# Kernel tuning notes

Measured on AMD Instinct MI355X. Metric: run time of the kernel, lower is better.

Reference implementation:

```python
import jax, jax.numpy as jnp
import numpy as np

N, E, G = 50000, 800000, 128          # nodes, edges, graphs
L, T, F = 4, 4, 20                    # conv layers, towers, per-tower width
D = T * F                             # 80 = hidden dim
EDGE_DIM = 16
AVG_DEG_LOG = float(np.log(17.0))     # avg_deg['log'] for avg in-degree ~16
EPS_STD = 1e-5
EPS_BN = 1e-5


def setup_inputs() -> dict:
    ks = iter(jax.random.split(jax.random.key(0), 32))
    rn = lambda *s: jax.random.normal(next(ks), s, jnp.float32) * 0.1
    return dict(
        x=jax.random.randint(next(ks), (N, 9), 0, 16),
        edge_index=jax.random.randint(next(ks), (2, E), 0, N),
        batch=jnp.sort(jax.random.randint(next(ks), (N,), 0, G)),
        edge_attr=rn(E, EDGE_DIM),
        atom_emb=rn(9, 16, D),
        edge_w=rn(L, EDGE_DIM, F), edge_b=jnp.zeros((L, F), jnp.float32),
        pre_w1=rn(L, T, 3 * F, F), pre_b1=jnp.zeros((L, T, F), jnp.float32),
        pre_w2=rn(L, T, F, F), pre_b2=jnp.zeros((L, T, F), jnp.float32),
        post_w1=rn(L, T, 13 * F, F), post_b1=jnp.zeros((L, T, F), jnp.float32),
        post_w2=rn(L, T, F, F), post_b2=jnp.zeros((L, T, F), jnp.float32),
        lin_w=rn(L, D, D), lin_b=jnp.zeros((L, D), jnp.float32),
        bn_g=jnp.ones((L, D), jnp.float32), bn_b=jnp.zeros((L, D), jnp.float32),
        mlp_w1=rn(D, 40), mlp_b1=jnp.zeros(40, jnp.float32),
        mlp_w2=rn(40, 20), mlp_b2=jnp.zeros(20, jnp.float32),
        mlp_w3=rn(20, 1), mlp_b3=jnp.zeros(1, jnp.float32),
    )


def _net(x, edge_index, batch, edge_attr, atom_emb, edge_w, edge_b, pre_w1,
         pre_b1, pre_w2, pre_b2, post_w1, post_b1, post_w2, post_b2, lin_w,
         lin_b, bn_g, bn_b, mlp_w1, mlp_b1, mlp_w2, mlp_b2, mlp_w3, mlp_b3):
    src, dst = edge_index[0], edge_index[1]
    # AtomEncoder: sum of 9 categorical embeddings -> [N, D]
    h = atom_emb[jnp.arange(9)[None, :], x].sum(1)
    deg_raw = jax.ops.segment_sum(jnp.ones((E,), jnp.float32), dst, N)
    deg = jnp.clip(deg_raw, 1.0)
    has_edge = (deg_raw > 0)[:, None, None]
    d3 = deg[:, None, None]
    logd = jnp.log(deg + 1.0)[:, None, None]
    for l in range(L):  # 4 PNAConv + BN + ReLU + residual (dropout off / eval)
        xt = h.reshape(N, T, F)
        ea = edge_attr @ edge_w[l] + edge_b[l]                      # [E, F]
        # message: concat(x_i, x_j, edge) -> per-tower pre MLP
        m = jnp.concatenate([xt[dst], xt[src],
                             jnp.broadcast_to(ea[:, None, :], (E, T, F))], -1)
        m = jax.nn.relu(jnp.einsum('eti,tio->eto', m, pre_w1[l]) + pre_b1[l])
        m = jnp.einsum('eti,tio->eto', m, pre_w2[l]) + pre_b2[l]    # [E,T,F]
        # multi-aggregator scatter-reduce
        mean = jax.ops.segment_sum(m, dst, N) / d3
        msq = jax.ops.segment_sum(m * m, dst, N) / d3
        std = jnp.sqrt(jax.nn.relu(msq - mean * mean) + EPS_STD)
        mn = jnp.where(has_edge, jax.ops.segment_min(m, dst, N), 0.0)
        mx = jnp.where(has_edge, jax.ops.segment_max(m, dst, N), 0.0)
        agg = jnp.concatenate([mean, mn, mx, std], -1)              # [N,T,4F]
        # degree scalers: identity, amplification, attenuation
        out = jnp.concatenate([agg, agg * (logd / AVG_DEG_LOG),
                               agg * (AVG_DEG_LOG / logd)], -1)     # [N,T,12F]
        out = jnp.concatenate([xt, out], -1)                        # [N,T,13F]
        out = jax.nn.relu(jnp.einsum('nti,tio->nto', out, post_w1[l]) + post_b1[l])
        out = jnp.einsum('nti,tio->nto', out, post_w2[l]) + post_b2[l]
        out = out.reshape(N, D) @ lin_w[l] + lin_b[l]
        # BatchNorm over nodes (batch statistics)
        mu = out.mean(0)
        var = jnp.mean((out - mu) ** 2, axis=0)
        out = (out - mu) * (bn_g[l] / jnp.sqrt(var + EPS_BN)) + bn_b[l]
        h = jax.nn.relu(out) + h
    # global mean pool over graphs + readout MLP
    cnt = jnp.clip(jax.ops.segment_sum(jnp.ones((N,), jnp.float32), batch, G), 1.0)
    g = jax.ops.segment_sum(h, batch, G) / cnt[:, None]
    g = jax.nn.relu(g @ mlp_w1 + mlp_b1)
    g = jax.nn.relu(g @ mlp_w2 + mlp_b2)
    return g @ mlp_w3 + mlp_b3                                      # [G, 1]


def reference(x, edge_index, batch, edge_attr, atom_emb, edge_w, edge_b, pre_w1,
              pre_b1, pre_w2, pre_b2, post_w1, post_b1, post_w2, post_b2, lin_w,
              lin_b, bn_g, bn_b, mlp_w1, mlp_b1, mlp_w2, mlp_b2, mlp_w3, mlp_b3):
    return _net(x, edge_index, batch, edge_attr, atom_emb, edge_w, edge_b, pre_w1,
                pre_b1, pre_w2, pre_b2, post_w1, post_b1, post_w2, post_b2,
                lin_w, lin_b, bn_g, bn_b, mlp_w1, mlp_b1, mlp_w2, mlp_b2,
                mlp_w3, mlp_b3)
```

## Files before the change

kernel.cpp:

```cpp
#include <hip/hip_runtime.h>
#include <hip/hip_bf16.h>

#define NN 50000
#define EE 800000
#define GG 128
#define LL 4
#define TT 4
#define FF 20
#define DD 80
#define SCAN_B ((NN + 1023) / 1024)
#define TILE_N 16
#define ITEMS (TILE_N * 10)
static constexpr float AVG_LOG = 2.8332133440562162f;

typedef __fp16 half2v __attribute__((ext_vector_type(2)));

__device__ __forceinline__ float bf2f(unsigned short u) {
  return __uint_as_float((unsigned)u << 16);
}
__device__ __forceinline__ unsigned short f2bf(float f) {
  __hip_bfloat16 b = __float2bfloat16(f);
  return *(unsigned short*)&b;
}
__device__ __forceinline__ half2v pkrtz(float a, float b) {
#if __has_builtin(__builtin_amdgcn_cvt_pkrtz)
  return __builtin_amdgcn_cvt_pkrtz(a, b);
#else
  half2v h; h.x = (__fp16)a; h.y = (__fp16)b; return h;
#endif
}
__device__ __forceinline__ float fdot2(half2v a, half2v b, float c) {
#if __has_builtin(__builtin_amdgcn_fdot2)
  return __builtin_amdgcn_fdot2(a, b, c, false);
#else
  return fmaf((float)a.x, (float)b.x, fmaf((float)a.y, (float)b.y, c));
#endif
}
__device__ __forceinline__ half2v u2h2(unsigned int u) {
  return __builtin_bit_cast(half2v, u);
}
__device__ __forceinline__ unsigned int h22u(half2v h) {
  return __builtin_bit_cast(unsigned int, h);
}
__device__ __forceinline__ unsigned int packh2_rne(float a, float b) {
  half2v h; h.x = (__fp16)a; h.y = (__fp16)b;
  return h22u(h);
}
__device__ __forceinline__ unsigned int pack_bf16(float a, float b) {
  return (unsigned int)f2bf(a) | ((unsigned int)f2bf(b) << 16);
}

__global__ __launch_bounds__(256) void k_h(const int* __restrict__ x,
                                           const float* __restrict__ atom_emb,
                                           float* __restrict__ h) {
  int idx = blockIdx.x * 256 + threadIdx.x;
  if (idx >= NN * DD) return;
  int n = idx / DD, d = idx - n * DD;
  const int* xr = x + n * 9;
  float acc = 0.f;
#pragma unroll
  for (int i = 0; i < 9; ++i) {
    int v = xr[i];
    acc += atom_emb[(i * 16 + v) * DD + d];
  }
  h[idx] = acc;
}

__global__ __launch_bounds__(256) void k_deg(const int* __restrict__ ei, int* __restrict__ cnt) {
  int e = blockIdx.x * 256 + threadIdx.x;
  if (e >= EE) return;
  atomicAdd(&cnt[ei[EE + e]], 1);
}

__global__ __launch_bounds__(1024) void k_scan_sum(const int* __restrict__ cnt, int* __restrict__ bsum) {
  __shared__ int red[1024];
  int tid = threadIdx.x;
  int i = blockIdx.x * 1024 + tid;
  red[tid] = (i < NN) ? cnt[i] : 0;
  __syncthreads();
  for (int off = 512; off > 0; off >>= 1) {
    if (tid < off) red[tid] += red[tid + off];
    __syncthreads();
  }
  if (tid == 0) bsum[blockIdx.x] = red[0];
}

__global__ void k_scan_top(const int* __restrict__ bsum, int* __restrict__ boff,
                           int* __restrict__ row_ptr) {
  if (threadIdx.x == 0 && blockIdx.x == 0) {
    int acc = 0;
    for (int b = 0; b < SCAN_B; ++b) { boff[b] = acc; acc += bsum[b]; }
    row_ptr[NN] = acc;
  }
}

__global__ __launch_bounds__(1024) void k_scan_apply(const int* __restrict__ cnt,
                                                     const int* __restrict__ boff,
                                                     int* __restrict__ row_ptr,
                                                     int* __restrict__ cursor) {
  __shared__ int sm[1024];
  int tid = threadIdx.x;
  int i = blockIdx.x * 1024 + tid;
  int v = (i < NN) ? cnt[i] : 0;
  sm[tid] = v;
  __syncthreads();
  for (int off = 1; off < 1024; off <<= 1) {
    int t = (tid >= off) ? sm[tid - off] : 0;
    __syncthreads();
    sm[tid] += t;
    __syncthreads();
  }
  int excl = boff[blockIdx.x] + sm[tid] - v;
  if (i < NN) { row_ptr[i] = excl; cursor[i] = excl; }
}

__global__ __launch_bounds__(256) void k_csrfill(const int* __restrict__ ei,
                                                 int* __restrict__ cursor,
                                                 int* __restrict__ csr_src,
                                                 int* __restrict__ csr_eid,
                                                 int* __restrict__ csr_dst) {
  int e = blockIdx.x * 256 + threadIdx.x;
  if (e >= EE) return;
  int dst = ei[EE + e];
  int slot = atomicAdd(&cursor[dst], 1);
  csr_src[slot] = ei[e];
  csr_eid[slot] = e;
  csr_dst[slot] = dst;
}

__global__ __launch_bounds__(256) void k_eagather(const int* __restrict__ csr_eid,
                                                  const float* __restrict__ edge_attr,
                                                  unsigned int* __restrict__ ea16) {
  int sl = blockIdx.x * 256 + threadIdx.x;
  if (sl >= EE) return;
  int e = csr_eid[sl];
  const float4* ap = (const float4*)(edge_attr + (size_t)e * 16);
  uint4 o0, o1;
  float4 v0 = ap[0], v1 = ap[1], v2 = ap[2], v3 = ap[3];
  o0.x = packh2_rne(v0.x, v0.y); o0.y = packh2_rne(v0.z, v0.w);
  o0.z = packh2_rne(v1.x, v1.y); o0.w = packh2_rne(v1.z, v1.w);
  o1.x = packh2_rne(v2.x, v2.y); o1.y = packh2_rne(v2.z, v2.w);
  o1.z = packh2_rne(v3.x, v3.y); o1.w = packh2_rne(v3.z, v3.w);
  uint4* op = (uint4*)(ea16 + (size_t)sl * 8);
  op[0] = o0; op[1] = o1;
}

__global__ __launch_bounds__(256) void k_nodeparams(const int* __restrict__ cnt,
                                                    float* __restrict__ inv_deg,
                                                    float* __restrict__ s1a,
                                                    float* __restrict__ s2a) {
  int n = blockIdx.x * 256 + threadIdx.x;
  if (n >= NN) return;
  int c = cnt[n];
  float deg = (c > 0) ? (float)c : 1.0f;
  inv_deg[n] = 1.0f / deg;
  float logd = logf(deg + 1.0f);
  s1a[n] = logd / AVG_LOG;
  s2a[n] = AVG_LOG / logd;
}

__global__ __launch_bounds__(64) void k_wcomb(const float* __restrict__ edge_w,
                                              const float* __restrict__ edge_b,
                                              const float* __restrict__ pre_w1,
                                              const float* __restrict__ pre_b1,
                                              const float* __restrict__ pre_w2,
                                              unsigned int* __restrict__ wcpk,
                                              unsigned int* __restrict__ w2pk,
                                              float* __restrict__ biasc, int l) {
  int t = blockIdx.x;
  int wt = l * TT + t;
  const float* W1 = pre_w1 + (size_t)wt * 1200;
  const float* W2 = pre_w2 + (size_t)wt * 400;
  const float* ew = edge_w + (size_t)l * 16 * FF;
  const float* eb = edge_b + (size_t)l * FF;
  int j = threadIdx.x;
  if (j >= FF) return;
  float col[16];
  for (int i = 0; i < 16; ++i) {
    float acc = 0.f;
#pragma unroll
    for (int f = 0; f < FF; ++f) acc = fmaf(ew[i * FF + f], W1[(40 + f) * FF + j], acc);
    col[i] = acc;
  }
#pragma unroll
  for (int i2 = 0; i2 < 8; ++i2)
    wcpk[((size_t)t * FF + j) * 8 + i2] = packh2_rne(col[2 * i2], col[2 * i2 + 1]);
#pragma unroll
  for (int i2 = 0; i2 < 10; ++i2)
    w2pk[((size_t)t * FF + j) * 10 + i2] = packh2_rne(W2[(2 * i2) * FF + j], W2[(2 * i2 + 1) * FF + j]);
  float b = pre_b1[wt * FF + j];
#pragma unroll
  for (int f = 0; f < FF; ++f) b = fmaf(eb[f], W1[(40 + f) * FF + j], b);
  biasc[t * FF + j] = b;
}

__global__ __launch_bounds__(64) void k_postpk(const float* __restrict__ post_w1,
                                               const float* __restrict__ post_w2,
                                               unsigned int* __restrict__ q1pk,
                                               unsigned int* __restrict__ q2pk, int l) {
  int t = blockIdx.x;
  int wt = l * TT + t;
  const float* Q1 = post_w1 + (size_t)wt * 5200;
  const float* Q2 = post_w2 + (size_t)wt * 400;
  int j = threadIdx.x;
  if (j >= FF) return;
  for (int i2 = 0; i2 < 120; ++i2) {
    int blk = i2 / 40, k = i2 - blk * 40;
    int r0 = 20 + 80 * blk + 2 * k;
    q1pk[((size_t)t * 120 + i2) * FF + j] = packh2_rne(Q1[r0 * FF + j], Q1[(r0 + 1) * FF + j]);
  }
#pragma unroll
  for (int i2 = 0; i2 < 10; ++i2)
    q2pk[((size_t)t * 10 + i2) * FF + j] = packh2_rne(Q2[(2 * i2) * FF + j], Q2[(2 * i2 + 1) * FF + j]);
}

__global__ __launch_bounds__(256) void k_prenode(
    const float* __restrict__ h, const float* __restrict__ pre_w1,
    const float* __restrict__ biasc,
    unsigned short* __restrict__ predD, unsigned short* __restrict__ predS, int l) {
  int tid = threadIdx.x;
  int t = tid >> 6, lane = tid & 63;
  int n = blockIdx.x * 64 + lane;
  if (n >= NN) return;
  int wt_u = __builtin_amdgcn_readfirstlane(l * TT + t);
  const float* W1 = pre_w1 + (size_t)wt_u * 1200;
  const float* bc = biasc + t * FF;
  float xt[FF];
  {
    const float4* pp = (const float4*)(h + (size_t)n * DD + t * FF);
#pragma unroll
    for (int i = 0; i < 5; ++i) { float4 v = pp[i]; xt[i*4]=v.x; xt[i*4+1]=v.y; xt[i*4+2]=v.z; xt[i*4+3]=v.w; }
  }
  float d[FF], s[FF];
#pragma unroll
  for (int j = 0; j < FF; ++j) { d[j] = bc[j]; s[j] = 0.f; }
#pragma unroll
  for (int i = 0; i < FF; ++i) {
    float a = xt[i];
#pragma unroll
    for (int j = 0; j < FF; ++j) {
      d[j] = fmaf(a, W1[i * FF + j], d[j]);
      s[j] = fmaf(a, W1[(FF + i) * FF + j], s[j]);
    }
  }
  ushort4* pd = (ushort4*)(predD + (size_t)n * DD + t * FF);
  ushort4* ps = (ushort4*)(predS + (size_t)n * DD + t * FF);
#pragma unroll
  for (int i = 0; i < 5; ++i) {
    pd[i] = make_ushort4(f2bf(d[i*4]), f2bf(d[i*4+1]), f2bf(d[i*4+2]), f2bf(d[i*4+3]));
    ps[i] = make_ushort4(f2bf(s[i*4]), f2bf(s[i*4+1]), f2bf(s[i*4+2]), f2bf(s[i*4+3]));
  }
}

__global__ __launch_bounds__(256, 4) void k_preagg(
    const unsigned short* __restrict__ predD,
    const unsigned short* __restrict__ predS,
    const unsigned int* __restrict__ ea16,
    const int* __restrict__ csr_src,
    const int* __restrict__ csr_dst,
    const int* __restrict__ row_ptr,
    const float* __restrict__ inv_deg,
    const unsigned int* __restrict__ wcpk,
    const unsigned int* __restrict__ w2pk,
    const float* __restrict__ pre_b2,
    unsigned short* __restrict__ aggbuf,
    int l) {
  __shared__ int nbr[TILE_N + 1];
  __shared__ float dDs[TT][TILE_N * FF];
  __shared__ unsigned int m2w[TT][64 * 11];
  int tid = threadIdx.x;
  int t = tid >> 6, lane = tid & 63;
  int t_u = __builtin_amdgcn_readfirstlane(t);
  int n0 = blockIdx.x * TILE_N;
  const unsigned int* Wcp = wcpk + (size_t)t_u * FF * 8;
  const unsigned int* W2p = w2pk + (size_t)t_u * FF * 10;
  const float* b2 = pre_b2 + (size_t)(l * TT + t_u) * FF;

  if (tid <= TILE_N) {
    int node = n0 + tid; if (node > NN) node = NN;
    nbr[tid] = row_ptr[node];
  }
  for (int i = lane; i < TILE_N * FF; i += 64) {
    int ni = i / FF, ch = i - ni * FF;
    int node = n0 + ni;
    dDs[t][i] = (node < NN) ? bf2f(predD[(size_t)node * DD + t_u * FF + ch]) : 0.f;
  }
  __syncthreads();
  int tbeg = nbr[0], tend = nbr[TILE_N];

  int itN[3], itP[3], itB[3], itE[3];
#pragma unroll
  for (int k = 0; k < 3; ++k) {
    int it = lane + 64 * k;
    bool v = it < ITEMS;
    int nd = v ? (it / 10) : 0;
    itN[k] = nd;
    itP[k] = v ? (it - nd * 10) : 0;
    itB[k] = v ? nbr[nd] : 0;
    itE[k] = v ? nbr[nd + 1] : 0;
  }
  float sS[3][2], sQ[3][2], sN[3][2], sX[3][2];
#pragma unroll
  for (int k = 0; k < 3; ++k) {
    sS[k][0] = 0.f; sS[k][1] = 0.f; sQ[k][0] = 0.f; sQ[k][1] = 0.f;
    sN[k][0] = 3.4e38f; sN[k][1] = 3.4e38f; sX[k][0] = -3.4e38f; sX[k][1] = -3.4e38f;
  }

  for (int wb = tbeg; wb < tend; wb += 64) {
    int p = wb + lane;
    if (p < tend) {
      int src = csr_src[p];
      int ni = csr_dst[p] - n0;
      float m1[FF];
      {
        const float4* dd = (const float4*)(&dDs[t][ni * FF]);
        const ushort4* qq = (const ushort4*)(predS + (size_t)src * DD + t_u * FF);
#pragma unroll
        for (int i = 0; i < 5; ++i) {
          float4 d4 = dd[i];
          ushort4 v = qq[i];
          m1[i*4+0] = d4.x + bf2f(v.x);
          m1[i*4+1] = d4.y + bf2f(v.y);
          m1[i*4+2] = d4.z + bf2f(v.z);
          m1[i*4+3] = d4.w + bf2f(v.w);
        }
      }
      half2v eap[8];
      {
        const uint4* ep = (const uint4*)(ea16 + (size_t)p * 8);
        uint4 e0 = ep[0], e1 = ep[1];
        eap[0] = u2h2(e0.x); eap[1] = u2h2(e0.y); eap[2] = u2h2(e0.z); eap[3] = u2h2(e0.w);
        eap[4] = u2h2(e1.x); eap[5] = u2h2(e1.y); eap[6] = u2h2(e1.z); eap[7] = u2h2(e1.w);
      }
#pragma unroll
      for (int j = 0; j < FF; ++j) {
        float c = m1[j];
#pragma unroll
        for (int i2 = 0; i2 < 8; ++i2) c = fdot2(eap[i2], u2h2(Wcp[j * 8 + i2]), c);
        m1[j] = c;
      }
      half2v mp[10];
#pragma unroll
      for (int pr = 0; pr < 10; ++pr)
        mp[pr] = pkrtz(fmaxf(m1[2*pr], 0.f), fmaxf(m1[2*pr+1], 0.f));
      float m2[FF];
#pragma unroll
      for (int j = 0; j < FF; ++j) {
        float c = b2[j];
#pragma unroll
        for (int i2 = 0; i2 < 10; ++i2) c = fdot2(mp[i2], u2h2(W2p[j * 10 + i2]), c);
        m2[j] = c;
      }
      unsigned int* row = &m2w[t][lane * 11];
#pragma unroll
      for (int pr = 0; pr < 10; ++pr) row[pr] = h22u(pkrtz(m2[2*pr], m2[2*pr+1]));
    }
    __syncthreads();
    int we = (wb + 64 < tend) ? (wb + 64) : tend;
#pragma unroll
    for (int k = 0; k < 3; ++k) {
      int lo = itB[k] > wb ? itB[k] : wb;
      int hi = itE[k] < we ? itE[k] : we;
      for (int s = lo; s < hi; ++s) {
        half2v h2 = u2h2(m2w[t][(s - wb) * 11 + itP[k]]);
        float v0 = (float)h2.x, v1 = (float)h2.y;
        sS[k][0] += v0; sQ[k][0] = fmaf(v0, v0, sQ[k][0]);
        sN[k][0] = fminf(sN[k][0], v0); sX[k][0] = fmaxf(sX[k][0], v0);
        sS[k][1] += v1; sQ[k][1] = fmaf(v1, v1, sQ[k][1]);
        sN[k][1] = fminf(sN[k][1], v1); sX[k][1] = fmaxf(sX[k][1], v1);
      }
    }
    __syncthreads();
  }

#pragma unroll
  for (int k = 0; k < 3; ++k) {
    int it = lane + 64 * k;
    if (it < ITEMS) {
      int n = n0 + itN[k];
      if (n < NN) {
        float inv = inv_deg[n];
        bool noe = (itE[k] <= itB[k]);
        float mu0 = sS[k][0] * inv, mu1 = sS[k][1] * inv;
        float sd0 = sqrtf(fmaxf(sQ[k][0] * inv - mu0 * mu0, 0.f) + 1e-5f);
        float sd1 = sqrtf(fmaxf(sQ[k][1] * inv - mu1 * mu1, 0.f) + 1e-5f);
        float mn0 = noe ? 0.f : sN[k][0], mn1 = noe ? 0.f : sN[k][1];
        float mx0 = noe ? 0.f : sX[k][0], mx1 = noe ? 0.f : sX[k][1];
        unsigned short* ab = aggbuf + ((size_t)n * 4 + t_u) * 80;
        ((unsigned int*)(ab))[itP[k]]      = pack_bf16(mu0, mu1);
        ((unsigned int*)(ab + 20))[itP[k]] = pack_bf16(mn0, mn1);
        ((unsigned int*)(ab + 40))[itP[k]] = pack_bf16(mx0, mx1);
        ((unsigned int*)(ab + 60))[itP[k]] = pack_bf16(sd0, sd1);
      }
    }
  }
}

__global__ __launch_bounds__(256) void k_postlin(
    const float* __restrict__ h, const unsigned short* __restrict__ aggbuf,
    const float* __restrict__ s1a, const float* __restrict__ s2a,
    const float* __restrict__ post_w1, const float* __restrict__ post_b1,
    const unsigned int* __restrict__ q1pk, const unsigned int* __restrict__ q2pk,
    const float* __restrict__ post_b2,
    const float* __restrict__ lin_w, const float* __restrict__ lin_b,
    float* __restrict__ outl, float* __restrict__ colsum, int l) {
  __shared__ float Wl[DD * DD];
  __shared__ float rows[DD * 65];
  int tid = threadIdx.x;
  int t = tid >> 6, lane = tid & 63;
  int t_u = __builtin_amdgcn_readfirstlane(t);
  int wt_u = __builtin_amdgcn_readfirstlane(l * TT + t);
  int n = blockIdx.x * 64 + lane;

  {
    const float4* src = (const float4*)(lin_w + (size_t)l * DD * DD);
    float4* dst = (float4*)Wl;
    for (int i = tid; i < DD * DD / 4; i += 256) dst[i] = src[i];
  }

  const float* Q1 = post_w1 + (size_t)wt_u * 5200;
  const float* B1 = post_b1 + (size_t)wt_u * FF;
  const float* B2 = post_b2 + (size_t)wt_u * FF;
  const unsigned int* q1 = q1pk + (size_t)t_u * 120 * FF;
  const unsigned int* q2 = q2pk + (size_t)t_u * 10 * FF;
  if (n < NN) {
    float c1 = s1a[n], c2 = s2a[n];
    half2v c1p = pkrtz(c1, c1), c2p = pkrtz(c2, c2);
    float xt[FF];
    {
      const float4* pp = (const float4*)(h + (size_t)n * DD + t_u * FF);
#pragma unroll
      for (int i = 0; i < 5; ++i) { float4 v = pp[i]; xt[i*4]=v.x; xt[i*4+1]=v.y; xt[i*4+2]=v.z; xt[i*4+3]=v.w; }
    }
    half2v a0p[40];
    {
      const uint4* ap = (const uint4*)(aggbuf + ((size_t)n * 4 + t_u) * 80);
#pragma unroll
      for (int q = 0; q < 10; ++q) {
        uint4 v = ap[q];
        unsigned int w[4] = {v.x, v.y, v.z, v.w};
#pragma unroll
        for (int k = 0; k < 4; ++k) {
          unsigned int u = w[k];
          float lo = __uint_as_float(u << 16);
          float hi = __uint_as_float(u & 0xffff0000u);
          a0p[q * 4 + k] = pkrtz(lo, hi);
        }
      }
    }
    float o1[FF];
#pragma unroll
    for (int j = 0; j < FF; ++j) o1[j] = B1[j];
#pragma unroll
    for (int i = 0; i < FF; ++i) {
      float a = xt[i];
#pragma unroll
      for (int j = 0; j < FF; ++j) o1[j] = fmaf(a, Q1[i * FF + j], o1[j]);
    }
#pragma unroll 2
    for (int k = 0; k < 40; ++k) {
      half2v act = a0p[k];
      const unsigned int* wr = q1 + k * FF;
#pragma unroll
      for (int j = 0; j < FF; ++j) o1[j] = fdot2(act, u2h2(wr[j]), o1[j]);
    }
#pragma unroll 2
    for (int k = 0; k < 40; ++k) {
      half2v act = a0p[k] * c1p;
      const unsigned int* wr = q1 + (40 + k) * FF;
#pragma unroll
      for (int j = 0; j < FF; ++j) o1[j] = fdot2(act, u2h2(wr[j]), o1[j]);
    }
#pragma unroll 2
    for (int k = 0; k < 40; ++k) {
      half2v act = a0p[k] * c2p;
      const unsigned int* wr = q1 + (80 + k) * FF;
#pragma unroll
      for (int j = 0; j < FF; ++j) o1[j] = fdot2(act, u2h2(wr[j]), o1[j]);
    }
    half2v o1p[10];
#pragma unroll
    for (int i2 = 0; i2 < 10; ++i2)
      o1p[i2] = pkrtz(fmaxf(o1[2*i2], 0.f), fmaxf(o1[2*i2+1], 0.f));
    float o2[FF];
#pragma unroll
    for (int j = 0; j < FF; ++j) o2[j] = B2[j];
#pragma unroll 2
    for (int i2 = 0; i2 < 10; ++i2) {
      half2v act = o1p[i2];
      const unsigned int* wr = q2 + i2 * FF;
#pragma unroll
      for (int j = 0; j < FF; ++j) o2[j] = fdot2(act, u2h2(wr[j]), o2[j]);
    }
#pragma unroll
    for (int j = 0; j < FF; ++j) rows[lane * DD + t_u * FF + j] = o2[j];
  } else {
#pragma unroll
    for (int j = 0; j < FF; ++j) rows[lane * DD + t_u * FF + j] = 0.f;
  }
  __syncthreads();

  int nl = tid >> 2;
  int d0 = (tid & 3) * FF;
  int n2 = blockIdx.x * 64 + nl;
  float acc[FF];
#pragma unroll
  for (int j = 0; j < FF; ++j) acc[j] = lin_b[l * DD + d0 + j];
  for (int i = 0; i < DD; ++i) {
    float r = rows[nl * DD + i];
    const float* wl = &Wl[i * DD + d0];
#pragma unroll
    for (int j = 0; j < FF; ++j) acc[j] = fmaf(r, wl[j], acc[j]);
  }
  if (n2 < NN) {
    float4* op = (float4*)(outl + (size_t)n2 * DD + d0);
#pragma unroll
    for (int i = 0; i < 5; ++i) op[i] = make_float4(acc[i*4], acc[i*4+1], acc[i*4+2], acc[i*4+3]);
  }
  __syncthreads();

  bool valid = (n2 < NN);
#pragma unroll
  for (int j = 0; j < FF; ++j) rows[(d0 + j) * 65 + nl] = valid ? acc[j] : 0.f;
  __syncthreads();
  if (tid < DD) {
    float s = 0.f;
    for (int k = 0; k < 64; ++k) s += rows[tid * 65 + k];
    atomicAdd(&colsum[tid], s);
  }
  __syncthreads();
#pragma unroll
  for (int j = 0; j < FF; ++j) rows[(d0 + j) * 65 + nl] = valid ? acc[j] * acc[j] : 0.f;
  __syncthreads();
  if (tid < DD) {
    float s = 0.f;
    for (int k = 0; k < 64; ++k) s += rows[tid * 65 + k];
    atomicAdd(&colsum[DD + tid], s);
  }
}

__global__ __launch_bounds__(128) void k_bnfinal(const float* __restrict__ colsum,
                                                 const float* __restrict__ bn_g,
                                                 const float* __restrict__ bn_b,
                                                 float* __restrict__ bnsc, int l) {
  int d = threadIdx.x;
  if (d >= DD) return;
  float mu = colsum[d] * (1.0f / NN);
  float var = colsum[DD + d] * (1.0f / NN) - mu * mu;
  float sc = bn_g[l * DD + d] * rsqrtf(var + 1e-5f);
  bnsc[d] = sc;
  bnsc[DD + d] = bn_b[l * DD + d] - mu * sc;
}

__global__ __launch_bounds__(256) void k_bnapply(const float* __restrict__ outl,
                                                 const float* __restrict__ bnsc,
                                                 float* __restrict__ h) {
  int idx = blockIdx.x * 256 + threadIdx.x;
  if (idx >= NN * DD) return;
  int d = idx % DD;
  float v = fmaf(outl[idx], bnsc[d], bnsc[DD + d]);
  h[idx] += fmaxf(v, 0.f);
}

__global__ __launch_bounds__(256) void k_gcnt(const int* __restrict__ batch, int* __restrict__ gcnt) {
  __shared__ int hcnt[GG];
  int tid = threadIdx.x;
  if (tid < GG) hcnt[tid] = 0;
  __syncthreads();
  int n = blockIdx.x * 256 + tid;
  if (n < NN) atomicAdd(&hcnt[batch[n]], 1);
  __syncthreads();
  if (tid < GG && hcnt[tid] > 0) atomicAdd(&gcnt[tid], hcnt[tid]);
}

__global__ void k_gstart(const int* __restrict__ gcnt, int* __restrict__ gstart) {
  if (threadIdx.x == 0 && blockIdx.x == 0) {
    int acc = 0;
    for (int g = 0; g < GG; ++g) { gstart[g] = acc; acc += gcnt[g]; }
  }
}

__global__ __launch_bounds__(320) void k_gmean(const float* __restrict__ h,
                                               const int* __restrict__ gstart,
                                               const int* __restrict__ gcnt,
                                               float* __restrict__ gbuf) {
  __shared__ float red[320];
  int g = blockIdx.x, tid = threadIdx.x;
  int nl = tid / DD, d = tid - nl * DD;
  int start = gstart[g], c = gcnt[g];
  float acc = 0.f;
  for (int r = start + nl; r < start + c; r += 4) acc += h[(size_t)r * DD + d];
  red[tid] = acc;
  __syncthreads();
  if (tid < DD) {
    float s = red[tid] + red[tid + DD] + red[tid + 2 * DD] + red[tid + 3 * DD];
    float cf = (c > 0) ? (float)c : 1.0f;
    gbuf[g * DD + tid] = s / cf;
  }
}

__global__ __launch_bounds__(64) void k_mlp(const float* __restrict__ gbuf,
                                            const float* __restrict__ w1, const float* __restrict__ b1,
                                            const float* __restrict__ w2, const float* __restrict__ b2,
                                            const float* __restrict__ w3, const float* __restrict__ b3,
                                            float* __restrict__ out) {
  __shared__ float row[DD];
  __shared__ float t1[40];
  __shared__ float t2[20];
  int g = blockIdx.x, tid = threadIdx.x;
  for (int i = tid; i < DD; i += 64) row[i] = gbuf[g * DD + i];
  __syncthreads();
  if (tid < 40) {
    float acc = b1[tid];
#pragma unroll
    for (int i = 0; i < DD; ++i) acc = fmaf(row[i], w1[i * 40 + tid], acc);
    t1[tid] = fmaxf(acc, 0.f);
  }
  __syncthreads();
  if (tid < 20) {
    float acc = b2[tid];
#pragma unroll
    for (int i = 0; i < 40; ++i) acc = fmaf(t1[i], w2[i * 20 + tid], acc);
    t2[tid] = fmaxf(acc, 0.f);
  }
  __syncthreads();
  if (tid == 0) {
    float acc = b3[0];
#pragma unroll
    for (int i = 0; i < 20; ++i) acc = fmaf(t2[i], w3[i], acc);
    out[g] = acc;
  }
}

extern "C" void kernel_launch(void* const* d_in, const int* in_sizes, int n_in,
                              void* d_out, int out_size, void* d_ws, size_t ws_size,
                              hipStream_t stream) {
  const int*   x         = (const int*)d_in[0];
  const int*   ei        = (const int*)d_in[1];
  const int*   batch     = (const int*)d_in[2];
  const float* edge_attr = (const float*)d_in[3];
  const float* atom_emb  = (const float*)d_in[4];
  const float* edge_w    = (const float*)d_in[5];
  const float* edge_b    = (const float*)d_in[6];
  const float* pre_w1    = (const float*)d_in[7];
  const float* pre_b1    = (const float*)d_in[8];
  const float* pre_w2    = (const float*)d_in[9];
  const float* pre_b2    = (const float*)d_in[10];
  const float* post_w1   = (const float*)d_in[11];
  const float* post_b1   = (const float*)d_in[12];
  const float* post_w2   = (const float*)d_in[13];
  const float* post_b2   = (const float*)d_in[14];
  const float* lin_w     = (const float*)d_in[15];
  const float* lin_b     = (const float*)d_in[16];
  const float* bn_g      = (const float*)d_in[17];
  const float* bn_b      = (const float*)d_in[18];
  const float* mlp_w1    = (const float*)d_in[19];
  const float* mlp_b1    = (const float*)d_in[20];
  const float* mlp_w2    = (const float*)d_in[21];
  const float* mlp_b2    = (const float*)d_in[22];
  const float* mlp_w3    = (const float*)d_in[23];
  const float* mlp_b3    = (const float*)d_in[24];
  float* out = (float*)d_out;

  char* ws = (char*)d_ws;
  size_t off = 0;
  auto alloc = [&](size_t bytes) -> void* {
    void* p = ws + off;
    off += (bytes + 15) & ~(size_t)15;
    return p;
  };
  float* h       = (float*)alloc((size_t)NN * DD * 4);
  float* outl    = (float*)alloc((size_t)NN * DD * 4);
  unsigned short* predD = (unsigned short*)alloc((size_t)NN * DD * 2);
  unsigned short* predS = (unsigned short*)alloc((size_t)NN * DD * 2);
  int*   csr_src = (int*)alloc((size_t)EE * 4);
  int*   csr_eid = (int*)alloc((size_t)EE * 4);
  int*   csr_dst = (int*)alloc((size_t)EE * 4);
  unsigned int* ea16 = (unsigned int*)alloc((size_t)EE * 8 * 4);
  int*   row_ptr = (int*)alloc((size_t)(NN + 1) * 4);
  int*   cnt     = (int*)alloc((size_t)NN * 4);
  int*   cursor  = (int*)alloc((size_t)NN * 4);
  float* inv_deg = (float*)alloc((size_t)NN * 4);
  float* s1a     = (float*)alloc((size_t)NN * 4);
  float* s2a     = (float*)alloc((size_t)NN * 4);
  float* colsum  = (float*)alloc(2 * DD * 4);
  float* bnsc    = (float*)alloc(2 * DD * 4);
  float* gbuf    = (float*)alloc((size_t)GG * DD * 4);
  unsigned int* wcpk  = (unsigned int*)alloc((size_t)TT * FF * 8 * 4);
  unsigned int* w2pk  = (unsigned int*)alloc((size_t)TT * FF * 10 * 4);
  unsigned int* q1pk  = (unsigned int*)alloc((size_t)TT * 120 * FF * 4);
  unsigned int* q2pk  = (unsigned int*)alloc((size_t)TT * 10 * FF * 4);
  float* biasc   = (float*)alloc((size_t)TT * FF * 4);
  int*   bsum    = (int*)alloc((size_t)SCAN_B * 4);
  int*   boff    = (int*)alloc((size_t)SCAN_B * 4);
  int*   gcnt    = (int*)alloc((size_t)GG * 4);
  int*   gstart  = (int*)alloc((size_t)(GG + 1) * 4);
  unsigned short* aggbuf = (unsigned short*)alloc((size_t)NN * 4 * 80 * 2);
  (void)in_sizes; (void)n_in; (void)out_size; (void)ws_size;

  hipMemsetAsync(cnt, 0, (size_t)NN * 4, stream);
  k_h<<<(NN * DD + 255) / 256, 256, 0, stream>>>(x, atom_emb, h);
  k_deg<<<(EE + 255) / 256, 256, 0, stream>>>(ei, cnt);
  k_scan_sum<<<SCAN_B, 1024, 0, stream>>>(cnt, bsum);
  k_scan_top<<<1, 64, 0, stream>>>(bsum, boff, row_ptr);
  k_scan_apply<<<SCAN_B, 1024, 0, stream>>>(cnt, boff, row_ptr, cursor);
  k_csrfill<<<(EE + 255) / 256, 256, 0, stream>>>(ei, cursor, csr_src, csr_eid, csr_dst);
  k_eagather<<<(EE + 255) / 256, 256, 0, stream>>>(csr_eid, edge_attr, ea16);
  k_nodeparams<<<(NN + 255) / 256, 256, 0, stream>>>(cnt, inv_deg, s1a, s2a);

  int tilesA = (NN + TILE_N - 1) / TILE_N;
  int blocksPL = (NN + 63) / 64;
  for (int l = 0; l < LL; ++l) {
    k_wcomb<<<TT, 64, 0, stream>>>(edge_w, edge_b, pre_w1, pre_b1, pre_w2, wcpk, w2pk, biasc, l);
    k_postpk<<<TT, 64, 0, stream>>>(post_w1, post_w2, q1pk, q2pk, l);
    k_prenode<<<(NN + 63) / 64, 256, 0, stream>>>(h, pre_w1, biasc, predD, predS, l);
    k_preagg<<<tilesA, 256, 0, stream>>>(predD, predS, ea16, csr_src, csr_dst, row_ptr,
        inv_deg, wcpk, w2pk, pre_b2, aggbuf, l);
    hipMemsetAsync(colsum, 0, 2 * DD * 4, stream);
    k_postlin<<<blocksPL, 256, 0, stream>>>(h, aggbuf, s1a, s2a,
        post_w1, post_b1, q1pk, q2pk, post_b2, lin_w, lin_b, outl, colsum, l);
    k_bnfinal<<<1, 128, 0, stream>>>(colsum, bn_g, bn_b, bnsc, l);
    k_bnapply<<<(NN * DD + 255) / 256, 256, 0, stream>>>(outl, bnsc, h);
  }

  hipMemsetAsync(gcnt, 0, (size_t)GG * 4, stream);
  k_gcnt<<<(NN + 255) / 256, 256, 0, stream>>>(batch, gcnt);
  k_gstart<<<1, 64, 0, stream>>>(gcnt, gstart);
  k_gmean<<<GG, 320, 0, stream>>>(h, gstart, gcnt, gbuf);
  k_mlp<<<GG, 64, 0, stream>>>(gbuf, mlp_w1, mlp_b1, mlp_w2, mlp_b2, mlp_w3, mlp_b3, out);
}
```

Baseline: 1.447 ms.

## Merge per-layer weight packing, drop BN finalize launch, read lin_w from global

Folds k_postpk into k_wcomb, which now also zeroes colsum, so the memset goes away. Folds the BN finalize into every bnapply block, each of which recomputes the scale and offset. Together these remove three small launches per layer. k_postlin no longer stages the 80x80 lin_w in shared memory: each wave computes its own tower's 20 output columns for its 64 nodes and reads lin_w from global/cache with wave-uniform addresses. This cuts LDS use and raises occupancy, at the cost of more cache loads and redundant BN math per block.

```diff
diff --git a/kernel.cpp b/kernel.cpp
--- a/kernel.cpp
+++ b/kernel.cpp
@@ -164,17 +164,25 @@
                                               const float* __restrict__ pre_w1,
                                               const float* __restrict__ pre_b1,
                                               const float* __restrict__ pre_w2,
+                                              const float* __restrict__ post_w1,
+                                              const float* __restrict__ post_w2,
                                               unsigned int* __restrict__ wcpk,
                                               unsigned int* __restrict__ w2pk,
-                                              float* __restrict__ biasc, int l) {
+                                              unsigned int* __restrict__ q1pk,
+                                              unsigned int* __restrict__ q2pk,
+                                              float* __restrict__ biasc,
+                                              float* __restrict__ colsum, int l) {
   int t = blockIdx.x;
   int wt = l * TT + t;
+  int j = threadIdx.x;
+  if (t == 0) {
+    for (int i = threadIdx.x; i < 2 * DD; i += 64) colsum[i] = 0.f;
+  }
+  if (j >= FF) return;
   const float* W1 = pre_w1 + (size_t)wt * 1200;
   const float* W2 = pre_w2 + (size_t)wt * 400;
   const float* ew = edge_w + (size_t)l * 16 * FF;
   const float* eb = edge_b + (size_t)l * FF;
-  int j = threadIdx.x;
-  if (j >= FF) return;
   float col[16];
   for (int i = 0; i < 16; ++i) {
     float acc = 0.f;
@@ -192,18 +200,8 @@
 #pragma unroll
   for (int f = 0; f < FF; ++f) b = fmaf(eb[f], W1[(40 + f) * FF + j], b);
   biasc[t * FF + j] = b;
-}
-
-__global__ __launch_bounds__(64) void k_postpk(const float* __restrict__ post_w1,
-                                               const float* __restrict__ post_w2,
-                                               unsigned int* __restrict__ q1pk,
-                                               unsigned int* __restrict__ q2pk, int l) {
-  int t = blockIdx.x;
-  int wt = l * TT + t;
   const float* Q1 = post_w1 + (size_t)wt * 5200;
   const float* Q2 = post_w2 + (size_t)wt * 400;
-  int j = threadIdx.x;
-  if (j >= FF) return;
   for (int i2 = 0; i2 < 120; ++i2) {
     int blk = i2 / 40, k = i2 - blk * 40;
     int r0 = 20 + 80 * blk + 2 * k;
@@ -404,19 +402,12 @@
     const float* __restrict__ post_b2,
     const float* __restrict__ lin_w, const float* __restrict__ lin_b,
     float* __restrict__ outl, float* __restrict__ colsum, int l) {
-  __shared__ float Wl[DD * DD];
-  __shared__ float rows[DD * 65];
+  __shared__ float rows[5280];
   int tid = threadIdx.x;
   int t = tid >> 6, lane = tid & 63;
   int t_u = __builtin_amdgcn_readfirstlane(t);
   int wt_u = __builtin_amdgcn_readfirstlane(l * TT + t);
   int n = blockIdx.x * 64 + lane;
-
-  {
-    const float4* src = (const float4*)(lin_w + (size_t)l * DD * DD);
-    float4* dst = (float4*)Wl;
-    for (int i = tid; i < DD * DD / 4; i += 256) dst[i] = src[i];
-  }
 
   const float* Q1 = post_w1 + (size_t)wt_u * 5200;
   const float* B1 = post_b1 + (size_t)wt_u * FF;
@@ -493,72 +484,70 @@
       for (int j = 0; j < FF; ++j) o2[j] = fdot2(act, u2h2(wr[j]), o2[j]);
     }
 #pragma unroll
-    for (int j = 0; j < FF; ++j) rows[lane * DD + t_u * FF + j] = o2[j];
+    for (int j = 0; j < FF; ++j) rows[lane * 81 + t_u * FF + j] = o2[j];
   } else {
 #pragma unroll
-    for (int j = 0; j < FF; ++j) rows[lane * DD + t_u * FF + j] = 0.f;
-  }
-  __syncthreads();
-
-  int nl = tid >> 2;
-  int d0 = (tid & 3) * FF;
-  int n2 = blockIdx.x * 64 + nl;
+    for (int j = 0; j < FF; ++j) rows[lane * 81 + t_u * FF + j] = 0.f;
+  }
+  __syncthreads();
+
+  int n2 = blockIdx.x * 64 + lane;
+  const float* WlG = lin_w + (size_t)l * DD * DD + t_u * FF;
   float acc[FF];
 #pragma unroll
-  for (int j = 0; j < FF; ++j) acc[j] = lin_b[l * DD + d0 + j];
+  for (int j = 0; j < FF; ++j) acc[j] = lin_b[l * DD + t_u * FF + j];
   for (int i = 0; i < DD; ++i) {
-    float r = rows[nl * DD + i];
-    const float* wl = &Wl[i * DD + d0];
+    float r = rows[lane * 81 + i];
+    const float* wl = WlG + i * DD;
 #pragma unroll
     for (int j = 0; j < FF; ++j) acc[j] = fmaf(r, wl[j], acc[j]);
   }
-  if (n2 < NN) {
-    float4* op = (float4*)(outl + (size_t)n2 * DD + d0);
+  bool valid = (n2 < NN);
+  if (valid) {
+    float4* op = (float4*)(outl + (size_t)n2 * DD + t_u * FF);
 #pragma unroll
     for (int i = 0; i < 5; ++i) op[i] = make_float4(acc[i*4], acc[i*4+1], acc[i*4+2], acc[i*4+3]);
   }
   __syncthreads();
 
-  bool valid = (n2 < NN);
-#pragma unroll
-  for (int j = 0; j < FF; ++j) rows[(d0 + j) * 65 + nl] = valid ? acc[j] : 0.f;
+#pragma unroll
+  for (int j = 0; j < FF; ++j) rows[(t_u * FF + j) * 66 + lane] = valid ? acc[j] : 0.f;
   __syncthreads();
   if (tid < DD) {
     float s = 0.f;
-    for (int k = 0; k < 64; ++k) s += rows[tid * 65 + k];
+    for (int k = 0; k < 64; ++k) s += rows[tid * 66 + k];
     atomicAdd(&colsum[tid], s);
   }
   __syncthreads();
 #pragma unroll
-  for (int j = 0; j < FF; ++j) rows[(d0 + j) * 65 + nl] = valid ? acc[j] * acc[j] : 0.f;
+  for (int j = 0; j < FF; ++j) rows[(t_u * FF + j) * 66 + lane] = valid ? acc[j] * acc[j] : 0.f;
   __syncthreads();
   if (tid < DD) {
     float s = 0.f;
-    for (int k = 0; k < 64; ++k) s += rows[tid * 65 + k];
+    for (int k = 0; k < 64; ++k) s += rows[tid * 66 + k];
     atomicAdd(&colsum[DD + tid], s);
   }
 }
 
-__global__ __launch_bounds__(128) void k_bnfinal(const float* __restrict__ colsum,
+__global__ __launch_bounds__(256) void k_bnapply(const float* __restrict__ outl,
+                                                 const float* __restrict__ colsum,
                                                  const float* __restrict__ bn_g,
                                                  const float* __restrict__ bn_b,
-                                                 float* __restrict__ bnsc, int l) {
-  int d = threadIdx.x;
-  if (d >= DD) return;
-  float mu = colsum[d] * (1.0f / NN);
-  float var = colsum[DD + d] * (1.0f / NN) - mu * mu;
-  float sc = bn_g[l * DD + d] * rsqrtf(var + 1e-5f);
-  bnsc[d] = sc;
-  bnsc[DD + d] = bn_b[l * DD + d] - mu * sc;
-}
-
-__global__ __launch_bounds__(256) void k_bnapply(const float* __restrict__ outl,
-                                                 const float* __restrict__ bnsc,
-                                                 float* __restrict__ h) {
-  int idx = blockIdx.x * 256 + threadIdx.x;
+                                                 float* __restrict__ h, int l) {
+  __shared__ float sc[DD], ofs[DD];
+  int tid = threadIdx.x;
+  if (tid < DD) {
+    float mu = colsum[tid] * (1.0f / NN);
+    float var = colsum[DD + tid] * (1.0f / NN) - mu * mu;
+    float s = bn_g[l * DD + tid] * rsqrtf(var + 1e-5f);
+    sc[tid] = s;
+    ofs[tid] = bn_b[l * DD + tid] - mu * s;
+  }
+  __syncthreads();
+  int idx = blockIdx.x * 256 + tid;
   if (idx >= NN * DD) return;
   int d = idx % DD;
-  float v = fmaf(outl[idx], bnsc[d], bnsc[DD + d]);
+  float v = fmaf(outl[idx], sc[d], ofs[d]);
   h[idx] += fmaxf(v, 0.f);
 }
 
@@ -684,7 +673,6 @@
   float* s1a     = (float*)alloc((size_t)NN * 4);
   float* s2a     = (float*)alloc((size_t)NN * 4);
   float* colsum  = (float*)alloc(2 * DD * 4);
-  float* bnsc    = (float*)alloc(2 * DD * 4);
   float* gbuf    = (float*)alloc((size_t)GG * DD * 4);
   unsigned int* wcpk  = (unsigned int*)alloc((size_t)TT * FF * 8 * 4);
   unsigned int* w2pk  = (unsigned int*)alloc((size_t)TT * FF * 10 * 4);
@@ -711,16 +699,14 @@
   int tilesA = (NN + TILE_N - 1) / TILE_N;
   int blocksPL = (NN + 63) / 64;
   for (int l = 0; l < LL; ++l) {
-    k_wcomb<<<TT, 64, 0, stream>>>(edge_w, edge_b, pre_w1, pre_b1, pre_w2, wcpk, w2pk, biasc, l);
-    k_postpk<<<TT, 64, 0, stream>>>(post_w1, post_w2, q1pk, q2pk, l);
+    k_wcomb<<<TT, 64, 0, stream>>>(edge_w, edge_b, pre_w1, pre_b1, pre_w2,
+        post_w1, post_w2, wcpk, w2pk, q1pk, q2pk, biasc, colsum, l);
     k_prenode<<<(NN + 63) / 64, 256, 0, stream>>>(h, pre_w1, biasc, predD, predS, l);
     k_preagg<<<tilesA, 256, 0, stream>>>(predD, predS, ea16, csr_src, csr_dst, row_ptr,
         inv_deg, wcpk, w2pk, pre_b2, aggbuf, l);
-    hipMemsetAsync(colsum, 0, 2 * DD * 4, stream);
     k_postlin<<<blocksPL, 256, 0, stream>>>(h, aggbuf, s1a, s2a,
         post_w1, post_b1, q1pk, q2pk, post_b2, lin_w, lin_b, outl, colsum, l);
-    k_bnfinal<<<1, 128, 0, stream>>>(colsum, bn_g, bn_b, bnsc, l);
-    k_bnapply<<<(NN * DD + 255) / 256, 256, 0, stream>>>(outl, bnsc, h);
+    k_bnapply<<<(NN * DD + 255) / 256, 256, 0, stream>>>(outl, colsum, bn_g, bn_b, h, l);
   }
 
   hipMemsetAsync(gcnt, 0, (size_t)GG * 4, stream);
```

Result: faster. 1.416 ms (-2.2%).
